# Kernel optimization log

Measured on AMD Instinct MI355X. Metric: run time of the kernel, lower is better.

The kernel has to match this reference:

```python
import jax, jax.numpy as jnp
import numpy as np

B, T, D, W, H = 64, 512, 768, 255, 8
DH = D // H

def layernorm(x, g, b, eps=1e-5):
    m = jnp.mean(x, axis=-1, keepdims=True)
    v = jnp.mean((x - m) ** 2, axis=-1, keepdims=True)
    return (x - m) * jax.lax.rsqrt(v + eps) * g + b

def setup_inputs() -> dict:
    key = jax.random.key(0)
    ks = list(jax.random.split(key, 12))
    p = lambda k, shape, s=0.02: (jax.random.normal(k, shape, jnp.float32) * s)
    # words_ids: -100 at CLS/SEP, each word spans 2 subtokens -> 255 words/row
    wi = np.full((B, T), -100, dtype=np.int32)
    pos = np.arange(1, T - 1)
    wi[:, 1:T - 1] = (pos - 1) // 2
    return {
        'output_bert': jax.random.normal(ks[0], (B, T, D), jnp.float32),
        'words_ids': jnp.asarray(wi),
        'Wq': p(ks[1], (D, D)), 'bq': jnp.zeros((D,), jnp.float32),
        'Wk': p(ks[2], (D, D)), 'bk': jnp.zeros((D,), jnp.float32),
        'Wv': p(ks[3], (D, D)), 'bv': jnp.zeros((D,), jnp.float32),
        'Wo': p(ks[4], (D, D)), 'bo': jnp.zeros((D,), jnp.float32),
        'ln1_g': jnp.ones((D,), jnp.float32), 'ln1_b': jnp.zeros((D,), jnp.float32),
        'W1f': p(ks[5], (D, 4 * D)), 'b1f': jnp.zeros((4 * D,), jnp.float32),
        'W2f': p(ks[6], (4 * D, D)), 'b2f': jnp.zeros((D,), jnp.float32),
        'ln2_g': jnp.ones((D,), jnp.float32), 'ln2_b': jnp.zeros((D,), jnp.float32),
        'ng': jnp.ones((D,), jnp.float32), 'nb': jnp.zeros((D,), jnp.float32),
        'lin_w': p(ks[7], (D, 2)), 'lin_b': jnp.zeros((2,), jnp.float32),
    }

def reference(output_bert, words_ids, Wq, bq, Wk, bk, Wv, bv, Wo, bo,
              ln1_g, ln1_b, W1f, b1f, W2f, b2f, ln2_g, ln2_b, ng, nb, lin_w, lin_b):
    Bsz = output_bert.shape[0]
    # --- first-subtoken gather: first token position of each word id ---
    hits = words_ids[:, None, :] == jnp.arange(W)[None, :, None]   # [B, W, T]
    first_idx = jnp.argmax(hits, axis=-1)                           # [B, W]
    feat = jnp.take_along_axis(output_bert, first_idx[..., None], axis=1)  # [B, W, D]
    # --- transformer encoder layer (post-norm, relu FFN) ---
    q = (feat @ Wq + bq).reshape(Bsz, W, H, DH)
    k = (feat @ Wk + bk).reshape(Bsz, W, H, DH)
    v = (feat @ Wv + bv).reshape(Bsz, W, H, DH)
    scores = jnp.einsum('bqhd,bkhd->bhqk', q, k) * (1.0 / np.sqrt(DH))
    attn = jax.nn.softmax(scores, axis=-1)
    ctx = jnp.einsum('bhqk,bkhd->bqhd', attn, v).reshape(Bsz, W, D)
    x = layernorm(feat + ctx @ Wo + bo, ln1_g, ln1_b)
    ff = jax.nn.relu(x @ W1f + b1f) @ W2f + b2f
    x = layernorm(x + ff, ln2_g, ln2_b)
    # --- final LayerNorm + Linear + softmax + argmax path ---
    x = layernorm(x, ng, nb)
    logits = x @ lin_w + lin_b
    ner_prob = jax.nn.softmax(logits, axis=-1)
    path = jnp.argmax(ner_prob, axis=-1)
    return ner_prob, path
```

## Files before the change

### kernel.cpp

```cpp
#include <hip/hip_runtime.h>
#include <cmath>

#define Bsz 64
#define Tt  512
#define Dd  768
#define Wn  255
#define Hh  8
#define DHd 96
#define NROWS (Bsz*Wn)

typedef _Float16 half_t;
typedef _Float16 f16x8 __attribute__((ext_vector_type(8)));
typedef _Float16 f16x4 __attribute__((ext_vector_type(4)));
typedef float f32x4 __attribute__((ext_vector_type(4)));

#define OFF_QKV_H 0
#define OFF_QKV_L 1769472
#define OFF_WO_H 3538944
#define OFF_WO_L 4128768
#define OFF_W1_H 4718592
#define OFF_W1_L 7077888
#define OFF_W2_H 9437184
#define OFF_W2_L 11796480
#define SLOTH 25165824
__device__ __align__(16) half_t g_w16[14155776];

__device__ __forceinline__ void gload16(const half_t* g, half_t* l) {
    __builtin_amdgcn_global_load_lds((const __attribute__((address_space(1))) void*)g,
                                     (__attribute__((address_space(3))) void*)l, 16, 0, 0);
}


__global__ void k_init_fi(int* fi) {
    int i = blockIdx.x * 256 + threadIdx.x;
    if (i < Bsz * Wn) fi[i] = 0x7fffffff;
}

__global__ void k_scan(const int* __restrict__ wid, int* __restrict__ fi) {
    int i = blockIdx.x * 256 + threadIdx.x;
    if (i >= Bsz * Tt) return;
    int b = i / Tt, t = i % Tt;
    int w = wid[i];
    if (w >= 0 && w < Wn) atomicMin(&fi[b * Wn + w], t);
}

__global__ void k_bcat(const float* __restrict__ bq, const float* __restrict__ bk,
                       const float* __restrict__ bv, float* __restrict__ o) {
    int i = blockIdx.x * 256 + threadIdx.x;
    if (i < 768) o[i] = bq[i];
    else if (i < 1536) o[i] = bk[i - 768];
    else if (i < 2304) o[i] = bv[i - 1536];
}

__global__ void k_gather(const float4* __restrict__ ob, const int* __restrict__ fi,
                         half_t* __restrict__ f16) {
    int i = blockIdx.x * 256 + threadIdx.x;
    if (i >= NROWS * 192) return;
    int r = i / 192, c = i % 192;
    int b = r / Wn;
    int idx = fi[r];
    if (idx == 0x7fffffff) idx = 0;
    float4 v = ob[((size_t)b * Tt + idx) * 192 + c];
    float a0 = v.x * 16.f, a1 = v.y * 16.f, a2 = v.z * 16.f, a3 = v.w * 16.f;
    half_t h0 = (half_t)a0, h1 = (half_t)a1, h2 = (half_t)a2, h3 = (half_t)a3;
    f16x4 hv = {h0, h1, h2, h3};
    f16x4 lv = {(half_t)(a0 - (float)h0), (half_t)(a1 - (float)h1),
                (half_t)(a2 - (float)h2), (half_t)(a3 - (float)h3)};
    size_t off = (size_t)r * 1536 + c * 4;
    *(f16x4*)&f16[off] = hv;
    *(f16x4*)&f16[off + 768] = lv;
}


__global__ void k_wsplit(const float* __restrict__ Wm, int K, int N,
                         size_t off_h, size_t off_l) {
    __shared__ float sm[32][33];
    const int tx = threadIdx.x, ty = threadIdx.y;
    const int n0 = blockIdx.x * 32, k0 = blockIdx.y * 32;
    #pragma unroll
    for (int r = 0; r < 4; ++r)
        sm[ty + r * 8][tx] = Wm[(size_t)(k0 + ty + r * 8) * N + n0 + tx];
    __syncthreads();
    half_t* oh = g_w16 + off_h;
    half_t* ol = g_w16 + off_l;
    #pragma unroll
    for (int r = 0; r < 4; ++r) {
        float v = 64.f * sm[tx][ty + r * 8];
        half_t hi = (half_t)v;
        size_t o = (size_t)(n0 + ty + r * 8) * K + k0 + tx;
        oh[o] = hi;
        ol[o] = (half_t)(v - (float)hi);
    }
}


template<int MODE, int AMODE, int NTILE>
__global__ __launch_bounds__(256, NTILE == 64 ? 3 : 2) void k_gemm16(
    const half_t* __restrict__ Ah, const half_t* __restrict__ Al, int lda,
    size_t boff_h, size_t boff_l,
    const float* __restrict__ bias,
    const void* __restrict__ res,
    void* __restrict__ out0, void* __restrict__ out1,
    int M, int N, int K) {
    constexpr int MI = (NTILE == 128 ? 4 : 2);
    __shared__ half_t sA[2][128 * 32];
    __shared__ half_t sB[2][NTILE * 32];
    const int tid = threadIdx.x;
    const int w = tid >> 6, l = tid & 63;
    int lin = blockIdx.y * gridDim.x + blockIdx.x;
    int rpx = gridDim.y >> 3;
    int j_ = lin >> 3;
    int jr = j_ / gridDim.x;
    int by = (lin & 7) * rpx + jr;
    int bx = j_ - jr * gridDim.x;
    const int row0 = by * 128, col0 = bx * NTILE;
    const half_t* Bh = g_w16 + boff_h;
    const half_t* Bl = g_w16 + boff_l;

    const int srow = l >> 2;
    const int skk  = (l & 3) * 8;
    const int fr = l & 15, qk = (l >> 4) * 8;
    const int mh = (NTILE == 128) ? (w >> 1) * 64 : w * 32;
    const int nh = (NTILE == 128) ? (w & 1) * 64 : 0;

    f32x4 acc[MI][4];
    #pragma unroll
    for (int i = 0; i < MI; ++i)
        #pragma unroll
        for (int j = 0; j < 4; ++j) acc[i][j] = (f32x4){0.f, 0.f, 0.f, 0.f};

    for (int k0 = 0; k0 < K; k0 += 32) {
        #pragma unroll
        for (int t = 0; t < 2; ++t) {
            int r = (w * 2 + t) * 16 + srow;
            int grA = row0 + r; if (grA >= M) grA = M - 1;
            half_t* da  = (half_t*)&sA[0][(w * 2 + t) * 512];
            half_t* da2 = (half_t*)&sA[1][(w * 2 + t) * 512];
            if (AMODE == 1) {
                int b = grA / 255, wl = grA - b * 255;
                int kk = k0 + skk;
                int h = kk / 96, d = kk - h * 96;
                size_t aoff = ((size_t)(b * 8 + h) * 256 + wl) * 192 + d;
                gload16(Ah + aoff, da);
                gload16(Al + aoff, da2);
            } else {
                gload16(Ah + (size_t)grA * lda + k0 + skk, da);
                gload16(Al + (size_t)grA * lda + k0 + skk, da2);
            }
            if (NTILE == 128 || t == 0) {
                int bs = (NTILE == 128) ? (w * 2 + t) : w;
                int grB = col0 + bs * 16 + srow;
                gload16(Bh + (size_t)grB * K + k0 + skk, (half_t*)&sB[0][bs * 512]);
                gload16(Bl + (size_t)grB * K + k0 + skk, (half_t*)&sB[1][bs * 512]);
            }
        }
        __syncthreads();
        f16x8 a0[MI], a1[MI], b0[4], b1[4];
        #pragma unroll
        for (int i = 0; i < MI; ++i) {
            a0[i] = *(const f16x8*)&sA[0][(mh + i * 16 + fr) * 32 + qk];
            a1[i] = *(const f16x8*)&sA[1][(mh + i * 16 + fr) * 32 + qk];
        }
        #pragma unroll
        for (int j = 0; j < 4; ++j) {
            b0[j] = *(const f16x8*)&sB[0][(nh + j * 16 + fr) * 32 + qk];
            b1[j] = *(const f16x8*)&sB[1][(nh + j * 16 + fr) * 32 + qk];
        }
        #pragma unroll
        for (int i = 0; i < MI; ++i)
            #pragma unroll
            for (int j = 0; j < 4; ++j) {
                acc[i][j] = __builtin_amdgcn_mfma_f32_16x16x32_f16(a0[i], b0[j], acc[i][j], 0, 0, 0);
                acc[i][j] = __builtin_amdgcn_mfma_f32_16x16x32_f16(a0[i], b1[j], acc[i][j], 0, 0, 0);
                acc[i][j] = __builtin_amdgcn_mfma_f32_16x16x32_f16(a1[i], b0[j], acc[i][j], 0, 0, 0);
            }
        __syncthreads();
    }

    const float dsc = 1.0f / 1024.0f;
    #pragma unroll
    for (int i = 0; i < MI; ++i) {
        #pragma unroll
        for (int r = 0; r < 4; ++r) {
            int row = row0 + mh + i * 16 + ((l >> 4) << 2) + r;
            if (row >= M) continue;
            #pragma unroll
            for (int j = 0; j < 4; ++j) {
                int col = col0 + nh + j * 16 + (l & 15);
                float vv = acc[i][j][r] * dsc + bias[col];
                if (MODE == 5) {
                    int b = row / 255, wl = row - b * 255;
                    int part = col / 768;
                    int cc = col - part * 768;
                    int h = cc / 96, d = cc - h * 96;
                    float t16 = vv * 16.f;
                    half_t hi = (half_t)t16;
                    half_t lo = (half_t)(t16 - (float)hi);
                    half_t* dst = (half_t*)out0 + (size_t)part * SLOTH;
                    size_t o = ((size_t)(b * 8 + h) * 256 + wl) * 192 + d;
                    dst[o] = hi; dst[o + 96] = lo;
                } else if (MODE == 1) {
                    const half_t* rp = (const half_t*)res;
                    vv += ((float)rp[(size_t)row * 1536 + col] +
                           (float)rp[(size_t)row * 1536 + 768 + col]) * 0.0625f;
                    ((float*)out0)[(size_t)row * N + col] = vv;
                } else if (MODE == 2) {
                    vv = fmaxf(vv, 0.f);
                    float t16 = vv * 16.f;
                    half_t hi = (half_t)t16;
                    ((half_t*)out0)[(size_t)row * N + col] = hi;
                    ((half_t*)out1)[(size_t)row * N + col] = (half_t)(t16 - (float)hi);
                } else {
                    vv += ((const float*)res)[(size_t)row * N + col];
                    ((float*)out0)[(size_t)row * N + col] = vv;
                }
            }
        }
    }
}


__global__ __launch_bounds__(256, 2) void k_attn2(half_t* __restrict__ qc,
                                                  const half_t* __restrict__ kk16,
                                                  const half_t* __restrict__ vv16) {
    __shared__ half_t sK[64][200];
    __shared__ half_t sVT[192][72];
    __shared__ float  sP[4][16][68];
    const int tid = threadIdx.x;
    const int w = tid >> 6, l = tid & 63;
    const int lr = l & 15, lc = l >> 4;
    const size_t base = (size_t)blockIdx.x * 49152;
    const float ssc = 0.10206207261596575f / 256.0f;

    for (int pass = 0; pass < 2; ++pass) {
        f32x4 O[2][6];
        float mrow[2][4], lrow[2][4];
        #pragma unroll
        for (int qs = 0; qs < 2; ++qs) {
            #pragma unroll
            for (int dn = 0; dn < 6; ++dn) O[qs][dn] = (f32x4){0.f, 0.f, 0.f, 0.f};
            #pragma unroll
            for (int r = 0; r < 4; ++r) { mrow[qs][r] = -3e38f; lrow[qs][r] = 0.f; }
        }
        for (int kt = 0; kt < 4; ++kt) {
            __syncthreads();
            #pragma unroll
            for (int c = 0; c < 6; ++c) {
                int ch = w + c * 4;
                *(f16x8*)&sK[l][ch * 8] =
                    *(const f16x8*)(kk16 + base + (size_t)(kt * 64 + l) * 192 + ch * 8);
            }
            #pragma unroll
            for (int c = 0; c < 6; ++c) {
                int ch = w + c * 4;
                f16x8 vv = *(const f16x8*)(vv16 + base + (size_t)(kt * 64 + l) * 192 + ch * 8);
                #pragma unroll
                for (int j = 0; j < 8; ++j) sVT[ch * 8 + j][l] = vv[j];
            }
            __syncthreads();
            #pragma unroll
            for (int qs = 0; qs < 2; ++qs) {
                const int qrow0 = (pass * 2 + qs) * 64 + w * 16;
                f16x8 qf0[3], qf1[3];
                #pragma unroll
                for (int s = 0; s < 3; ++s) {
                    qf0[s] = *(const f16x8*)(qc + base + (size_t)(qrow0 + lr) * 192 + s * 32 + lc * 8);
                    qf1[s] = *(const f16x8*)(qc + base + (size_t)(qrow0 + lr) * 192 + 96 + s * 32 + lc * 8);
                }
                f32x4 sacc[4];
                #pragma unroll
                for (int nt = 0; nt < 4; ++nt) sacc[nt] = (f32x4){0.f, 0.f, 0.f, 0.f};
                #pragma unroll
                for (int s = 0; s < 3; ++s)
                    #pragma unroll
                    for (int nt = 0; nt < 4; ++nt) {
                        f16x8 kh = *(const f16x8*)&sK[nt * 16 + lr][s * 32 + lc * 8];
                        f16x8 klo = *(const f16x8*)&sK[nt * 16 + lr][96 + s * 32 + lc * 8];
                        sacc[nt] = __builtin_amdgcn_mfma_f32_16x16x32_f16(qf0[s], kh, sacc[nt], 0, 0, 0);
                        sacc[nt] = __builtin_amdgcn_mfma_f32_16x16x32_f16(qf0[s], klo, sacc[nt], 0, 0, 0);
                        sacc[nt] = __builtin_amdgcn_mfma_f32_16x16x32_f16(qf1[s], kh, sacc[nt], 0, 0, 0);
                    }
                float sv[4][4], mx[4] = {-3e38f, -3e38f, -3e38f, -3e38f};
                #pragma unroll
                for (int nt = 0; nt < 4; ++nt) {
                    int key = kt * 64 + nt * 16 + lr;
                    #pragma unroll
                    for (int r = 0; r < 4; ++r) {
                        float s_ = sacc[nt][r] * ssc;
                        if (key >= 255) s_ = -3e38f;
                        sv[nt][r] = s_;
                        mx[r] = fmaxf(mx[r], s_);
                    }
                }
                #pragma unroll
                for (int r = 0; r < 4; ++r) {
                    mx[r] = fmaxf(mx[r], __shfl_xor(mx[r], 1));
                    mx[r] = fmaxf(mx[r], __shfl_xor(mx[r], 2));
                    mx[r] = fmaxf(mx[r], __shfl_xor(mx[r], 4));
                    mx[r] = fmaxf(mx[r], __shfl_xor(mx[r], 8));
                }
                float alpha[4], rsum[4];
                #pragma unroll
                for (int r = 0; r < 4; ++r) {
                    float mn = fmaxf(mrow[qs][r], mx[r]);
                    alpha[r] = __expf(mrow[qs][r] - mn);
                    mrow[qs][r] = mn;
                    rsum[r] = 0.f;
                }
                float pv[4][4];
                #pragma unroll
                for (int nt = 0; nt < 4; ++nt)
                    #pragma unroll
                    for (int r = 0; r < 4; ++r) {
                        float p = __expf(sv[nt][r] - mrow[qs][r]);
                        pv[nt][r] = p;
                        rsum[r] += p;
                    }
                #pragma unroll
                for (int r = 0; r < 4; ++r) {
                    rsum[r] += __shfl_xor(rsum[r], 1);
                    rsum[r] += __shfl_xor(rsum[r], 2);
                    rsum[r] += __shfl_xor(rsum[r], 4);
                    rsum[r] += __shfl_xor(rsum[r], 8);
                    lrow[qs][r] = lrow[qs][r] * alpha[r] + rsum[r];
                }
                #pragma unroll
                for (int dn = 0; dn < 6; ++dn)
                    #pragma unroll
                    for (int r = 0; r < 4; ++r) O[qs][dn][r] *= alpha[r];
                #pragma unroll
                for (int nt = 0; nt < 4; ++nt)
                    #pragma unroll
                    for (int r = 0; r < 4; ++r)
                        sP[w][lc * 4 + r][nt * 16 + lr] = pv[nt][r];
                #pragma unroll
                for (int ks = 0; ks < 2; ++ks) {
                    const float* pp = &sP[w][lr][ks * 32 + lc * 8];
                    f16x8 ph, pl;
                    #pragma unroll
                    for (int j = 0; j < 8; ++j) {
                        float p = pp[j];
                        half_t h_ = (half_t)p;
                        ph[j] = h_;
                        pl[j] = (half_t)(p - (float)h_);
                    }
                    #pragma unroll
                    for (int dn = 0; dn < 6; ++dn) {
                        f16x8 vh = *(const f16x8*)&sVT[dn * 16 + lr][ks * 32 + lc * 8];
                        f16x8 vl = *(const f16x8*)&sVT[96 + dn * 16 + lr][ks * 32 + lc * 8];
                        O[qs][dn] = __builtin_amdgcn_mfma_f32_16x16x32_f16(ph, vh, O[qs][dn], 0, 0, 0);
                        O[qs][dn] = __builtin_amdgcn_mfma_f32_16x16x32_f16(ph, vl, O[qs][dn], 0, 0, 0);
                        O[qs][dn] = __builtin_amdgcn_mfma_f32_16x16x32_f16(pl, vh, O[qs][dn], 0, 0, 0);
                    }
                }
            }
        }
        #pragma unroll
        for (int qs = 0; qs < 2; ++qs) {
            const int qrow0 = (pass * 2 + qs) * 64 + w * 16;
            #pragma unroll
            for (int r = 0; r < 4; ++r) {
                int qrow = qrow0 + lc * 4 + r;
                if (qrow >= Wn) continue;
                float inv = 1.0f / lrow[qs][r];
                #pragma unroll
                for (int dn = 0; dn < 6; ++dn) {
                    float val = O[qs][dn][r] * inv;
                    half_t hi = (half_t)val;
                    half_t lo = (half_t)(val - (float)hi);
                    size_t o = base + (size_t)qrow * 192 + dn * 16 + lr;
                    qc[o] = hi;
                    qc[o + 96] = lo;
                }
            }
        }
    }
}


template<int SPLIT>
__global__ __launch_bounds__(256) void k_ln(const float* __restrict__ X, const float* __restrict__ g,
                                            const float* __restrict__ bt, float* __restrict__ Y,
                                            half_t* __restrict__ Y16) {
    const int r = blockIdx.x, tid = threadIdx.x;
    __shared__ float red[256];
    const float* x = X + (size_t)r * Dd;
    float x0 = x[tid], x1 = x[tid + 256], x2 = x[tid + 512];
    red[tid] = x0 + x1 + x2; __syncthreads();
    for (int s = 128; s > 0; s >>= 1) { if (tid < s) red[tid] += red[tid + s]; __syncthreads(); }
    float mean = red[0] * (1.0f / 768.0f);
    __syncthreads();
    float d0 = x0 - mean, d1 = x1 - mean, d2 = x2 - mean;
    red[tid] = d0 * d0 + d1 * d1 + d2 * d2; __syncthreads();
    for (int s = 128; s > 0; s >>= 1) { if (tid < s) red[tid] += red[tid + s]; __syncthreads(); }
    float rs = rsqrtf(red[0] * (1.0f / 768.0f) + 1e-5f);
    float* y = Y + (size_t)r * Dd;
    float y0 = d0 * rs * g[tid]       + bt[tid];
    float y1 = d1 * rs * g[tid + 256] + bt[tid + 256];
    float y2 = d2 * rs * g[tid + 512] + bt[tid + 512];
    y[tid] = y0; y[tid + 256] = y1; y[tid + 512] = y2;
    if (SPLIT) {
        half_t* h = Y16 + (size_t)r * 1536;
        float t0 = y0 * 16.f, t1 = y1 * 16.f, t2 = y2 * 16.f;
        half_t h0 = (half_t)t0, h1 = (half_t)t1, h2 = (half_t)t2;
        h[tid] = h0; h[tid + 256] = h1; h[tid + 512] = h2;
        h[768 + tid] = (half_t)(t0 - (float)h0);
        h[768 + tid + 256] = (half_t)(t1 - (float)h1);
        h[768 + tid + 512] = (half_t)(t2 - (float)h2);
    }
}


__global__ __launch_bounds__(256) void k_final(const float* __restrict__ X, const float* __restrict__ g,
                                               const float* __restrict__ bt, const float* __restrict__ lw,
                                               const float* __restrict__ lb, float* __restrict__ out) {
    const int r = blockIdx.x, tid = threadIdx.x;
    __shared__ float red[256];
    const float* x = X + (size_t)r * Dd;
    float x0 = x[tid], x1 = x[tid + 256], x2 = x[tid + 512];
    red[tid] = x0 + x1 + x2; __syncthreads();
    for (int s = 128; s > 0; s >>= 1) { if (tid < s) red[tid] += red[tid + s]; __syncthreads(); }
    float mean = red[0] * (1.0f / 768.0f);
    __syncthreads();
    float d0 = x0 - mean, d1 = x1 - mean, d2 = x2 - mean;
    red[tid] = d0 * d0 + d1 * d1 + d2 * d2; __syncthreads();
    for (int s = 128; s > 0; s >>= 1) { if (tid < s) red[tid] += red[tid + s]; __syncthreads(); }
    float rs = rsqrtf(red[0] * (1.0f / 768.0f) + 1e-5f);
    __syncthreads();
    float n0 = d0 * rs * g[tid]       + bt[tid];
    float n1 = d1 * rs * g[tid + 256] + bt[tid + 256];
    float n2 = d2 * rs * g[tid + 512] + bt[tid + 512];
    float l0 = n0 * lw[2 * tid]     + n1 * lw[2 * (tid + 256)]     + n2 * lw[2 * (tid + 512)];
    float l1 = n0 * lw[2 * tid + 1] + n1 * lw[2 * (tid + 256) + 1] + n2 * lw[2 * (tid + 512) + 1];
    red[tid] = l0; __syncthreads();
    for (int s = 128; s > 0; s >>= 1) { if (tid < s) red[tid] += red[tid + s]; __syncthreads(); }
    l0 = red[0]; __syncthreads();
    red[tid] = l1; __syncthreads();
    for (int s = 128; s > 0; s >>= 1) { if (tid < s) red[tid] += red[tid + s]; __syncthreads(); }
    l1 = red[0];
    if (tid == 0) {
        l0 += lb[0]; l1 += lb[1];
        float m = fmaxf(l0, l1);
        float e0 = expf(l0 - m), e1 = expf(l1 - m);
        float inv = 1.0f / (e0 + e1);
        out[2 * r] = e0 * inv;
        out[2 * r + 1] = e1 * inv;
        out[2 * NROWS + r] = (l1 > l0) ? 1.0f : 0.0f;
    }
}


extern "C" void kernel_launch(void* const* d_in, const int* in_sizes, int n_in,
                              void* d_out, int out_size, void* d_ws, size_t ws_size,
                              hipStream_t stream) {
    const float* ob  = (const float*)d_in[0];
    const int*   wid = (const int*)d_in[1];
    const float* Wq  = (const float*)d_in[2];  const float* bq  = (const float*)d_in[3];
    const float* Wk  = (const float*)d_in[4];  const float* bk  = (const float*)d_in[5];
    const float* Wv  = (const float*)d_in[6];  const float* bv  = (const float*)d_in[7];
    const float* Wo  = (const float*)d_in[8];  const float* bo  = (const float*)d_in[9];
    const float* g1  = (const float*)d_in[10]; const float* b1  = (const float*)d_in[11];
    const float* W1f = (const float*)d_in[12]; const float* b1f = (const float*)d_in[13];
    const float* W2f = (const float*)d_in[14]; const float* b2f = (const float*)d_in[15];
    const float* g2  = (const float*)d_in[16]; const float* b2  = (const float*)d_in[17];
    const float* ng  = (const float*)d_in[18]; const float* nb  = (const float*)d_in[19];
    const float* lw  = (const float*)d_in[20]; const float* lb  = (const float*)d_in[21];
    float* out = (float*)d_out;

    char* ws = (char*)d_ws;
    const size_t MB = 1u << 20;
    const size_t SLOT = 48 * MB;
    int* fi = (int*)ws;
    float* bcat = (float*)(ws + 262144);
    char* S1 = ws + MB;
    char* S2 = S1 + SLOT;
    char* S3 = S2 + SLOT;
    char* S4 = S3 + SLOT;

    half_t* feat16 = (half_t*)S1;
    half_t* q16    = (half_t*)S2;
    half_t* k16    = (half_t*)S3;
    half_t* v16    = (half_t*)S4;
    float*  t1     = (float*)S3;
    float*  xbuf   = (float*)S4;
    half_t* x16    = (half_t*)S2;
    half_t* ffh_h  = (half_t*)S1;
    half_t* ffh_l  = (half_t*)S3;
    float*  t2     = (float*)S2;
    float*  x2     = (float*)S4;

    k_wsplit<<<dim3(24, 24), dim3(32, 8), 0, stream>>>(Wq, 768, 768, 0, 1769472);
    k_wsplit<<<dim3(24, 24), dim3(32, 8), 0, stream>>>(Wk, 768, 768, 589824, 2359296);
    k_wsplit<<<dim3(24, 24), dim3(32, 8), 0, stream>>>(Wv, 768, 768, 1179648, 2949120);
    k_wsplit<<<dim3(24, 24), dim3(32, 8), 0, stream>>>(Wo, 768, 768, OFF_WO_H, OFF_WO_L);
    k_wsplit<<<dim3(96, 24), dim3(32, 8), 0, stream>>>(W1f, 768, 3072, OFF_W1_H, OFF_W1_L);
    k_wsplit<<<dim3(24, 96), dim3(32, 8), 0, stream>>>(W2f, 3072, 768, OFF_W2_H, OFF_W2_L);
    k_bcat<<<9, 256, 0, stream>>>(bq, bk, bv, bcat);

    k_init_fi<<<(Bsz * Wn + 255) / 256, 256, 0, stream>>>(fi);
    k_scan<<<(Bsz * Tt) / 256, 256, 0, stream>>>(wid, fi);
    k_gather<<<(NROWS * 192 + 255) / 256, 256, 0, stream>>>((const float4*)ob, fi, feat16);

    k_gemm16<5, 0, 128><<<dim3(18, 128), 256, 0, stream>>>(
        feat16, feat16 + 768, 1536, OFF_QKV_H, OFF_QKV_L,
        bcat, nullptr, q16, nullptr, NROWS, 2304, Dd);

    k_attn2<<<Bsz * Hh, 256, 0, stream>>>(q16, k16, v16);

    k_gemm16<1, 1, 128><<<dim3(6, 128), 256, 0, stream>>>(
        q16, q16 + 96, 0, OFF_WO_H, OFF_WO_L,
        bo, feat16, t1, nullptr, NROWS, Dd, Dd);
    k_ln<1><<<NROWS, 256, 0, stream>>>(t1, g1, b1, xbuf, x16);

    for (int c = 0; c < 2; ++c) {
        const int r0 = c * 8160, mc = 8160;
        k_gemm16<2, 0, 128><<<dim3(24, 64), 256, 0, stream>>>(
            x16 + (size_t)r0 * 1536, x16 + (size_t)r0 * 1536 + 768, 1536,
            OFF_W1_H, OFF_W1_L, b1f, nullptr, ffh_h, ffh_l, mc, 3072, Dd);
        k_gemm16<3, 0, 64><<<dim3(12, 64), 256, 0, stream>>>(
            ffh_h, ffh_l, 3072, OFF_W2_H, OFF_W2_L, b2f, xbuf + (size_t)r0 * Dd,
            t2 + (size_t)r0 * Dd, nullptr, mc, Dd, 3072);
    }

    k_ln<0><<<NROWS, 256, 0, stream>>>(t2, g2, b2, x2, nullptr);
    k_final<<<NROWS, 256, 0, stream>>>(x2, ng, nb, lw, lb, out);
}
```

Baseline: 1.157 ms.

## Switch GEMM to 32x32x16 MFMA tiles and fuse final two layernorms

Rewrites the split-fp16 GEMM inner loop to use 32x32x16 MFMA instructions with 32x32 accumulator fragments instead of 16x16x32, which needs fewer LDS fragment loads per MFMA. The epilogue row and column mapping is adjusted to match. Launch bounds are raised to 3 waves for every tile size, which may force register spilling with 32-float accumulators. Separately, the second layernorm is fused into the final norm, linear and softmax kernel, removing one launch and an fp32 round trip through memory.

Result: slower. 1.333 ms (+15.2%).

```diff
diff --git a/kernel.cpp b/kernel.cpp
--- a/kernel.cpp
+++ b/kernel.cpp
@@ -13,6 +13,7 @@
 typedef _Float16 f16x8 __attribute__((ext_vector_type(8)));
 typedef _Float16 f16x4 __attribute__((ext_vector_type(4)));
 typedef float f32x4 __attribute__((ext_vector_type(4)));
+typedef float f32x16 __attribute__((ext_vector_type(16)));
 
 #define OFF_QKV_H 0
 #define OFF_QKV_L 1769472
@@ -95,14 +96,14 @@
 
 
 template<int MODE, int AMODE, int NTILE>
-__global__ __launch_bounds__(256, NTILE == 64 ? 3 : 2) void k_gemm16(
+__global__ __launch_bounds__(256, 3) void k_gemm16(
     const half_t* __restrict__ Ah, const half_t* __restrict__ Al, int lda,
     size_t boff_h, size_t boff_l,
     const float* __restrict__ bias,
     const void* __restrict__ res,
     void* __restrict__ out0, void* __restrict__ out1,
     int M, int N, int K) {
-    constexpr int MI = (NTILE == 128 ? 4 : 2);
+    constexpr int MI32 = (NTILE == 128 ? 2 : 1);
     __shared__ half_t sA[2][128 * 32];
     __shared__ half_t sB[2][NTILE * 32];
     const int tid = threadIdx.x;
@@ -119,15 +120,17 @@
 
     const int srow = l >> 2;
     const int skk  = (l & 3) * 8;
-    const int fr = l & 15, qk = (l >> 4) * 8;
+    const int m32 = l & 31, kh8 = (l >> 5) * 8;
     const int mh = (NTILE == 128) ? (w >> 1) * 64 : w * 32;
     const int nh = (NTILE == 128) ? (w & 1) * 64 : 0;
 
-    f32x4 acc[MI][4];
+    f32x16 acc[MI32][2];
     #pragma unroll
-    for (int i = 0; i < MI; ++i)
-        #pragma unroll
-        for (int j = 0; j < 4; ++j) acc[i][j] = (f32x4){0.f, 0.f, 0.f, 0.f};
+    for (int i = 0; i < MI32; ++i)
+        #pragma unroll
+        for (int j = 0; j < 2; ++j)
+            #pragma unroll
+            for (int r = 0; r < 16; ++r) acc[i][j][r] = 0.f;
 
     for (int k0 = 0; k0 < K; k0 += 32) {
         #pragma unroll
@@ -155,38 +158,44 @@
             }
         }
         __syncthreads();
-        f16x8 a0[MI], a1[MI], b0[4], b1[4];
-        #pragma unroll
-        for (int i = 0; i < MI; ++i) {
-            a0[i] = *(const f16x8*)&sA[0][(mh + i * 16 + fr) * 32 + qk];
-            a1[i] = *(const f16x8*)&sA[1][(mh + i * 16 + fr) * 32 + qk];
-        }
-        #pragma unroll
-        for (int j = 0; j < 4; ++j) {
-            b0[j] = *(const f16x8*)&sB[0][(nh + j * 16 + fr) * 32 + qk];
-            b1[j] = *(const f16x8*)&sB[1][(nh + j * 16 + fr) * 32 + qk];
-        }
-        #pragma unroll
-        for (int i = 0; i < MI; ++i)
-            #pragma unroll
-            for (int j = 0; j < 4; ++j) {
-                acc[i][j] = __builtin_amdgcn_mfma_f32_16x16x32_f16(a0[i], b0[j], acc[i][j], 0, 0, 0);
-                acc[i][j] = __builtin_amdgcn_mfma_f32_16x16x32_f16(a0[i], b1[j], acc[i][j], 0, 0, 0);
-                acc[i][j] = __builtin_amdgcn_mfma_f32_16x16x32_f16(a1[i], b0[j], acc[i][j], 0, 0, 0);
-            }
+        f16x8 a0[MI32][2], a1[MI32][2], b0[2][2], b1[2][2];
+        #pragma unroll
+        for (int i = 0; i < MI32; ++i)
+            #pragma unroll
+            for (int h = 0; h < 2; ++h) {
+                a0[i][h] = *(const f16x8*)&sA[0][(mh + i * 32 + m32) * 32 + h * 16 + kh8];
+                a1[i][h] = *(const f16x8*)&sA[1][(mh + i * 32 + m32) * 32 + h * 16 + kh8];
+            }
+        #pragma unroll
+        for (int j = 0; j < 2; ++j)
+            #pragma unroll
+            for (int h = 0; h < 2; ++h) {
+                b0[j][h] = *(const f16x8*)&sB[0][(nh + j * 32 + m32) * 32 + h * 16 + kh8];
+                b1[j][h] = *(const f16x8*)&sB[1][(nh + j * 32 + m32) * 32 + h * 16 + kh8];
+            }
+        #pragma unroll
+        for (int i = 0; i < MI32; ++i)
+            #pragma unroll
+            for (int j = 0; j < 2; ++j)
+                #pragma unroll
+                for (int h = 0; h < 2; ++h) {
+                    acc[i][j] = __builtin_amdgcn_mfma_f32_32x32x16_f16(a0[i][h], b0[j][h], acc[i][j], 0, 0, 0);
+                    acc[i][j] = __builtin_amdgcn_mfma_f32_32x32x16_f16(a0[i][h], b1[j][h], acc[i][j], 0, 0, 0);
+                    acc[i][j] = __builtin_amdgcn_mfma_f32_32x32x16_f16(a1[i][h], b0[j][h], acc[i][j], 0, 0, 0);
+                }
         __syncthreads();
     }
 
     const float dsc = 1.0f / 1024.0f;
     #pragma unroll
-    for (int i = 0; i < MI; ++i) {
-        #pragma unroll
-        for (int r = 0; r < 4; ++r) {
-            int row = row0 + mh + i * 16 + ((l >> 4) << 2) + r;
+    for (int i = 0; i < MI32; ++i) {
+        #pragma unroll
+        for (int r = 0; r < 16; ++r) {
+            int row = row0 + mh + i * 32 + (r & 3) + 8 * (r >> 2) + 4 * (l >> 5);
             if (row >= M) continue;
             #pragma unroll
-            for (int j = 0; j < 4; ++j) {
-                int col = col0 + nh + j * 16 + (l & 15);
+            for (int j = 0; j < 2; ++j) {
+                int col = col0 + nh + j * 32 + m32;
                 float vv = acc[i][j][r] * dsc + bias[col];
                 if (MODE == 5) {
                     int b = row / 255, wl = row - b * 255;
@@ -378,10 +387,9 @@
 }
 
 
-template<int SPLIT>
-__global__ __launch_bounds__(256) void k_ln(const float* __restrict__ X, const float* __restrict__ g,
-                                            const float* __restrict__ bt, float* __restrict__ Y,
-                                            half_t* __restrict__ Y16) {
+__global__ __launch_bounds__(256) void k_ln1(const float* __restrict__ X, const float* __restrict__ g,
+                                             const float* __restrict__ bt, float* __restrict__ Y,
+                                             half_t* __restrict__ Y16) {
     const int r = blockIdx.x, tid = threadIdx.x;
     __shared__ float red[256];
     const float* x = X + (size_t)r * Dd;
@@ -399,21 +407,21 @@
     float y1 = d1 * rs * g[tid + 256] + bt[tid + 256];
     float y2 = d2 * rs * g[tid + 512] + bt[tid + 512];
     y[tid] = y0; y[tid + 256] = y1; y[tid + 512] = y2;
-    if (SPLIT) {
-        half_t* h = Y16 + (size_t)r * 1536;
-        float t0 = y0 * 16.f, t1 = y1 * 16.f, t2 = y2 * 16.f;
-        half_t h0 = (half_t)t0, h1 = (half_t)t1, h2 = (half_t)t2;
-        h[tid] = h0; h[tid + 256] = h1; h[tid + 512] = h2;
-        h[768 + tid] = (half_t)(t0 - (float)h0);
-        h[768 + tid + 256] = (half_t)(t1 - (float)h1);
-        h[768 + tid + 512] = (half_t)(t2 - (float)h2);
-    }
-}
-
-
-__global__ __launch_bounds__(256) void k_final(const float* __restrict__ X, const float* __restrict__ g,
-                                               const float* __restrict__ bt, const float* __restrict__ lw,
-                                               const float* __restrict__ lb, float* __restrict__ out) {
+    half_t* h = Y16 + (size_t)r * 1536;
+    float t0 = y0 * 16.f, t1 = y1 * 16.f, t2 = y2 * 16.f;
+    half_t h0 = (half_t)t0, h1 = (half_t)t1, h2 = (half_t)t2;
+    h[tid] = h0; h[tid + 256] = h1; h[tid + 512] = h2;
+    h[768 + tid] = (half_t)(t0 - (float)h0);
+    h[768 + tid + 256] = (half_t)(t1 - (float)h1);
+    h[768 + tid + 512] = (half_t)(t2 - (float)h2);
+}
+
+
+__global__ __launch_bounds__(256) void k_final2(const float* __restrict__ X,
+                                                const float* __restrict__ g2, const float* __restrict__ b2,
+                                                const float* __restrict__ ng, const float* __restrict__ nb,
+                                                const float* __restrict__ lw, const float* __restrict__ lb,
+                                                float* __restrict__ out) {
     const int r = blockIdx.x, tid = threadIdx.x;
     __shared__ float red[256];
     const float* x = X + (size_t)r * Dd;
@@ -427,9 +435,21 @@
     for (int s = 128; s > 0; s >>= 1) { if (tid < s) red[tid] += red[tid + s]; __syncthreads(); }
     float rs = rsqrtf(red[0] * (1.0f / 768.0f) + 1e-5f);
     __syncthreads();
-    float n0 = d0 * rs * g[tid]       + bt[tid];
-    float n1 = d1 * rs * g[tid + 256] + bt[tid + 256];
-    float n2 = d2 * rs * g[tid + 512] + bt[tid + 512];
+    float y0 = d0 * rs * g2[tid]       + b2[tid];
+    float y1 = d1 * rs * g2[tid + 256] + b2[tid + 256];
+    float y2 = d2 * rs * g2[tid + 512] + b2[tid + 512];
+    red[tid] = y0 + y1 + y2; __syncthreads();
+    for (int s = 128; s > 0; s >>= 1) { if (tid < s) red[tid] += red[tid + s]; __syncthreads(); }
+    mean = red[0] * (1.0f / 768.0f);
+    __syncthreads();
+    float e0 = y0 - mean, e1 = y1 - mean, e2 = y2 - mean;
+    red[tid] = e0 * e0 + e1 * e1 + e2 * e2; __syncthreads();
+    for (int s = 128; s > 0; s >>= 1) { if (tid < s) red[tid] += red[tid + s]; __syncthreads(); }
+    rs = rsqrtf(red[0] * (1.0f / 768.0f) + 1e-5f);
+    __syncthreads();
+    float n0 = e0 * rs * ng[tid]       + nb[tid];
+    float n1 = e1 * rs * ng[tid + 256] + nb[tid + 256];
+    float n2 = e2 * rs * ng[tid + 512] + nb[tid + 512];
     float l0 = n0 * lw[2 * tid]     + n1 * lw[2 * (tid + 256)]     + n2 * lw[2 * (tid + 512)];
     float l1 = n0 * lw[2 * tid + 1] + n1 * lw[2 * (tid + 256) + 1] + n2 * lw[2 * (tid + 512) + 1];
     red[tid] = l0; __syncthreads();
@@ -441,10 +461,10 @@
     if (tid == 0) {
         l0 += lb[0]; l1 += lb[1];
         float m = fmaxf(l0, l1);
-        float e0 = expf(l0 - m), e1 = expf(l1 - m);
-        float inv = 1.0f / (e0 + e1);
-        out[2 * r] = e0 * inv;
-        out[2 * r + 1] = e1 * inv;
+        float e0_ = expf(l0 - m), e1_ = expf(l1 - m);
+        float inv = 1.0f / (e0_ + e1_);
+        out[2 * r] = e0_ * inv;
+        out[2 * r + 1] = e1_ * inv;
         out[2 * NROWS + r] = (l1 > l0) ? 1.0f : 0.0f;
     }
 }
@@ -487,7 +507,6 @@
     half_t* ffh_h  = (half_t*)S1;
     half_t* ffh_l  = (half_t*)S3;
     float*  t2     = (float*)S2;
-    float*  x2     = (float*)S4;
 
     k_wsplit<<<dim3(24, 24), dim3(32, 8), 0, stream>>>(Wq, 768, 768, 0, 1769472);
     k_wsplit<<<dim3(24, 24), dim3(32, 8), 0, stream>>>(Wk, 768, 768, 589824, 2359296);
@@ -510,7 +529,7 @@
     k_gemm16<1, 1, 128><<<dim3(6, 128), 256, 0, stream>>>(
         q16, q16 + 96, 0, OFF_WO_H, OFF_WO_L,
         bo, feat16, t1, nullptr, NROWS, Dd, Dd);
-    k_ln<1><<<NROWS, 256, 0, stream>>>(t1, g1, b1, xbuf, x16);
+    k_ln1<<<NROWS, 256, 0, stream>>>(t1, g1, b1, xbuf, x16);
 
     for (int c = 0; c < 2; ++c) {
         const int r0 = c * 8160, mc = 8160;
@@ -522,6 +541,5 @@
             t2 + (size_t)r0 * Dd, nullptr, mc, Dd, 3072);
     }
 
-    k_ln<0><<<NROWS, 256, 0, stream>>>(t2, g2, b2, x2, nullptr);
-    k_final<<<NROWS, 256, 0, stream>>>(x2, ng, nb, lw, lb, out);
-}
+    k_final2<<<NROWS, 256, 0, stream>>>(t2, g2, b2, ng, nb, lw, lb, out);
+}
```
